# Optimization experiments

Hardware: AMD Instinct MI355X
Metric: run time of the kernel (lower is better)

The kernel has to match this reference:

```python
import jax, jax.numpy as jnp
import numpy as np

B, T, V, E, H = 256, 512, 50000, 300, 128
NORM_GAIN = 0.8     # norm_gain fed at train time
FORGET_BIAS = 1.0
EPS = 1e-12         # tf.contrib.layers.layer_norm default epsilon


def setup_inputs() -> dict:
    key = jax.random.key(0)
    k1, k2, k3 = jax.random.split(key, 3)
    x = jax.random.randint(k1, (B, T), 0, V, dtype=jnp.int32)
    embed = jax.random.normal(k2, (V, E), dtype=jnp.float32)  # tf.random_normal stddev=1
    W = jax.random.normal(k3, (E + H, 4 * H), dtype=jnp.float32) / np.float32(np.sqrt(E + H))
    gains = jnp.full((5, H), NORM_GAIN, dtype=jnp.float32)   # i, j, f, o, cell-transform
    shifts = jnp.zeros((5, H), dtype=jnp.float32)
    return {"x": x, "embed": embed, "W": W, "gains": gains, "shifts": shifts}


def _ln(v, g, b):
    # layer norm over feature axis with learned gain/shift
    m = jnp.mean(v, axis=-1, keepdims=True)
    var = jnp.mean(jnp.square(v - m), axis=-1, keepdims=True)
    return (v - m) * jax.lax.rsqrt(var + EPS) * g + b


def reference(x, embed, W, gains, shifts):
    # embedding: einsum('abc,cd->abd', one_hot(x), embed) == embed[x]
    xe = jnp.take(embed, x, axis=0)            # [B, T, E]
    xe = jnp.transpose(xe, (1, 0, 2))          # [T, B, E] for scan
    c0 = jnp.zeros((x.shape[0], H), jnp.float32)
    h0 = c0

    def step(carry, x_t):
        c, h = carry
        z = jnp.concatenate([x_t, h], axis=-1) @ W      # [B, 4H], no bias
        i, j, f, o = jnp.split(z, 4, axis=-1)
        i = _ln(i, gains[0], shifts[0])
        j = _ln(j, gains[1], shifts[1])
        f = _ln(f, gains[2], shifts[2])
        o = _ln(o, gains[3], shifts[3])
        g = jax.nn.relu(j)                              # activation=tf.nn.relu
        new_c = c * jax.nn.sigmoid(f + FORGET_BIAS) + jax.nn.sigmoid(i) * g
        new_h = jax.nn.relu(_ln(new_c, gains[4], shifts[4])) * jax.nn.sigmoid(o)
        return (new_c, new_h), new_h

    _, ys = jax.lax.scan(step, (c0, h0), xe)            # ys: [T, B, H]
    return jnp.transpose(ys, (1, 0, 2))                 # [B, T, H]
```

## Files before the change

kernel.cpp:

```cpp
#include <hip/hip_runtime.h>
#include <math.h>

#define Bb   256
#define Tt   512
#define Vv   50000
#define Ee   300
#define Hh   128
#define G4   512
#define EPS  1e-12f
#define FBIAS 1.0f

typedef _Float16 half8 __attribute__((ext_vector_type(8)));
typedef float    f32x4 __attribute__((ext_vector_type(4)));

template <int CTRL>
__device__ inline float dpp_mov(float v) {
    return __int_as_float(
        __builtin_amdgcn_update_dpp(0, __float_as_int(v), CTRL, 0xF, 0xF, true));
}
__device__ inline float red16(float v) {
    v += dpp_mov<0xB1>(v);
    v += dpp_mov<0x4E>(v);
    v += dpp_mov<0x141>(v);
    v += dpp_mov<0x140>(v);
    return v;
}
__device__ inline float red64b(float v) {
    v = red16(v);
    v += dpp_mov<0x142>(v);
    v += dpp_mov<0x143>(v);
    return __int_as_float(__builtin_amdgcn_readlane(__float_as_int(v), 63));
}

__device__ inline void lds_barrier() {
    asm volatile("s_waitcnt lgkmcnt(0)" ::: "memory");
    __builtin_amdgcn_s_barrier();
}

__device__ inline float sigm(float v) {
    return __fdividef(1.0f, 1.0f + __expf(-v));
}

#define PROJ_TILES ((Vv + 31) / 32)

__global__ __launch_bounds__(512, 2) void embed_proj_mfma(
    const float* __restrict__ embed,
    const float* __restrict__ W,
    _Float16* __restrict__ P)
{
    __shared__ __align__(16) _Float16 A[32 * 320];

    const int tid  = threadIdx.x;
    const int wv   = tid >> 6;
    const int lane = tid & 63;
    const int p16  = lane & 15;
    const int gq   = lane >> 4;

    half8 bf[4][10];
    #pragma unroll
    for (int tt = 0; tt < 4; ++tt) {
        #pragma unroll
        for (int ks = 0; ks < 10; ++ks) {
            half8 h;
            #pragma unroll
            for (int j = 0; j < 8; ++j) {
                int k = ks * 32 + gq * 8 + j;
                h[j] = (k < Ee)
                     ? (_Float16)W[(size_t)k * G4 + wv * 64 + tt * 16 + p16]
                     : (_Float16)0.f;
            }
            bf[tt][ks] = h;
        }
    }

    char* const Ab = (char*)A;
    for (int i = tid; i < 32 * 10; i += 512) {
        int row = i / 10, m = i - row * 10;
        *(uint*)(Ab + ((row * 640 + 600 + m * 4) ^ ((row & 7) << 4))) = 0u;
    }
    __syncthreads();

    for (int mtile = blockIdx.x; mtile < PROJ_TILES; mtile += gridDim.x) {
        const int r0 = mtile * 32;

        for (int i = tid; i < 32 * 75; i += 512) {
            int row = i / 75, k4 = i - row * 75;
            int grow = r0 + row;
            float4 v = (grow < Vv) ? *(const float4*)&embed[(size_t)grow * Ee + k4 * 4]
                                   : (float4){0.f, 0.f, 0.f, 0.f};
            union { _Float16 h[4]; uint2 u; } pk;
            pk.h[0] = (_Float16)v.x; pk.h[1] = (_Float16)v.y;
            pk.h[2] = (_Float16)v.z; pk.h[3] = (_Float16)v.w;
            *(uint2*)(Ab + ((row * 640 + k4 * 8) ^ ((row & 7) << 4))) = pk.u;
        }
        __syncthreads();

        f32x4 acc[2][4];
        #pragma unroll
        for (int mt = 0; mt < 2; ++mt)
            #pragma unroll
            for (int tt = 0; tt < 4; ++tt)
                acc[mt][tt] = (f32x4){0.f, 0.f, 0.f, 0.f};

        #pragma unroll
        for (int mt = 0; mt < 2; ++mt) {
            const int arow = mt * 16 + p16;
            #pragma unroll
            for (int ks = 0; ks < 10; ++ks) {
                half8 af = *(const half8*)(Ab + ((arow * 640 + ks * 64 + gq * 16)
                                                 ^ ((arow & 7) << 4)));
                #pragma unroll
                for (int tt = 0; tt < 4; ++tt)
                    acc[mt][tt] = __builtin_amdgcn_mfma_f32_16x16x32_f16(
                        af, bf[tt][ks], acc[mt][tt], 0, 0, 0);
            }
        }

        #pragma unroll
        for (int mt = 0; mt < 2; ++mt)
            #pragma unroll
            for (int tt = 0; tt < 4; ++tt)
                #pragma unroll
                for (int r = 0; r < 4; ++r) {
                    int row = r0 + mt * 16 + gq * 4 + r;
                    if (row < Vv)
                        P[(size_t)row * G4 + wv * 64 + tt * 16 + p16] =
                            (_Float16)acc[mt][tt][r];
                }
        __syncthreads();
    }
}

__global__ __launch_bounds__(128) void wsum_kernel(
    const float* __restrict__ W, float* __restrict__ Wsum)
{
    const int k = threadIdx.x;
    const float* wr = W + (size_t)(Ee + k) * G4;
    #pragma unroll
    for (int g = 0; g < 4; ++g) {
        float s = 0.f;
        for (int c = 0; c < 128; c += 4) {
            float4 v = *(const float4*)&wr[g * 128 + c];
            s += (v.x + v.y) + (v.z + v.w);
        }
        Wsum[k * 4 + g] = s;
    }
}

__global__ __launch_bounds__(256) void psum_kernel(
    const _Float16* __restrict__ P, float* __restrict__ Psum)
{
    const int lane = threadIdx.x & 63;
    const int wid  = (blockIdx.x * 256 + threadIdx.x) >> 6;
    const int nw   = (gridDim.x * 256) >> 6;
    const int g    = lane >> 4;

    for (int row = wid; row < Vv; row += nw) {
        half8 v = *(const half8*)&P[(size_t)row * G4 + lane * 8];
        float s = 0.f;
        #pragma unroll
        for (int j = 0; j < 8; ++j) s += (float)v[j];
        s = red16(s);
        if ((lane & 15) == 0) Psum[row * 4 + g] = s;
    }
}

#define RPBLK 4
#define LBLK  (Bb / RPBLK)

#define LSTM_STEP(TSTEP, PC, QC, PL, QL)                                       \
{                                                                              \
              \
    {                                                                          \
        const _Float16* pr = P + (size_t)tkR * G4;                             \
        _Pragma("unroll")                                                      \
        for (int g = 0; g < 4; ++g)                                            \
            PL[g] = *(const uint*)&pr[g * 128 + 2 * lane];                     \
        QL = *(const float4*)&Psum[(size_t)tkR * 4];                           \
    }                                                                          \
    f32x4 acc_s = (f32x4){0.f, 0.f, 0.f, 0.f};                                 \
    {                                                                          \
        half8 af[4];                                                           \
        _Pragma("unroll")                                                      \
        for (int ks = 0; ks < 4; ++ks)                                         \
            af[ks] = *(const half8*)(hb + p16 * 256 +                          \
                         ((ks * 64 + (gq << 4)) ^ ((p16 & 7) << 4)));          \
        f32x4 acc[8];                                                          \
        _Pragma("unroll")                                                      \
        for (int tt = 0; tt < 8; ++tt) acc[tt] = (f32x4){0.f, 0.f, 0.f, 0.f};  \
        _Pragma("unroll")                                                      \
        for (int tt = 0; tt < 8; ++tt) {                                       \
            _Pragma("unroll")                                                  \
            for (int ks = 0; ks < 4; ++ks)                                     \
                acc[tt] = __builtin_amdgcn_mfma_f32_16x16x32_f16(              \
                    af[ks], bfrag[tt][ks], acc[tt], 0, 0, 0);                  \
        }                                                                      \
        _Pragma("unroll")                                                      \
        for (int ks = 0; ks < 4; ++ks)                                         \
            acc_s = __builtin_amdgcn_mfma_f32_16x16x32_f16(                    \
                af[ks], bsum[ks], acc_s, 0, 0, 0);                             \
        if (lane < 16) {                                                       \
            _Pragma("unroll")                                                  \
            for (int g = 0; g < 4; ++g) {                                      \
                _Pragma("unroll")                                              \
                for (int hh = 0; hh < 2; ++hh) {                               \
                    const int tt  = g * 2 + hh;                                \
                    const int col = g * 128 + wv * 32 + hh * 16 + p16;         \
                    _Pragma("unroll")                                          \
                    for (int r = 0; r < 4; ++r) z_lds[r][col] = acc[tt][r];    \
                }                                                              \
            }                                                                  \
        }                                                                      \
    }                                                                          \
    lds_barrier();                                               \
          \
    {                                                                          \
        tkR = xtok[wv][((TSTEP) + 4 < Tt) ? (TSTEP) + 4 : Tt - 1];             \
        float2 zi[4];                                                          \
        _Pragma("unroll")                                                      \
        for (int g = 0; g < 4; ++g) {                                          \
            union { uint u; _Float16 h[2]; } pk; pk.u = PC[g];                 \
            float2 zr = *(const float2*)&z_lds[wv][g * 128 + 2 * lane];        \
            zi[g].x = zr.x + (float)pk.h[0];                                   \
            zi[g].y = zr.y + (float)pk.h[1];                                   \
        }                                                                      \
              \
        float sr = acc_s[0];                                                   \
        sr = (wv == 1) ? acc_s[1] : sr;                                        \
        sr = (wv == 2) ? acc_s[2] : sr;                                        \
        sr = (wv == 3) ? acc_s[3] : sr;                                        \
        float mean[4], rstd[4];                                                \
        {                                                                      \
            const float qs[4] = {QC.x, QC.y, QC.z, QC.w};                      \
            _Pragma("unroll")                                                  \
            for (int g = 0; g < 4; ++g) {                                      \
                float sg_ = __int_as_float(                                    \
                    __builtin_amdgcn_readlane(__float_as_int(sr), g));         \
                mean[g] = (qs[g] + sg_) * (1.0f / Hh);                         \
            }                                                                  \
        }                                                                      \
        _Pragma("unroll")                                                      \
        for (int g = 0; g < 4; ++g) {                                          \
            float q = red64b(fmaf(zi[g].x, zi[g].x, zi[g].y * zi[g].y));       \
            float var = q * (1.0f / Hh) - mean[g] * mean[g];                   \
            rstd[g] = rsqrtf(var + EPS);                                       \
        }                                                                      \
        float2 nv[4];                                                          \
        _Pragma("unroll")                                                      \
        for (int g = 0; g < 4; ++g) {                                          \
            nv[g].x = (zi[g].x - mean[g]) * rstd[g] * gg[g].x + sg[g].x;       \
            nv[g].y = (zi[g].y - mean[g]) * rstd[g] * gg[g].y + sg[g].y;       \
        }                                                                      \
        const float sox = sigm(nv[3].x);                \
        const float soy = sigm(nv[3].y);                                       \
        c0 = c0 * sigm(nv[2].x + FBIAS) + sigm(nv[0].x) * fmaxf(nv[1].x, 0.f); \
        c1 = c1 * sigm(nv[2].y + FBIAS) + sigm(nv[0].y) * fmaxf(nv[1].y, 0.f); \
        float s2 = red64b(c0 + c1);                                            \
        float q2 = red64b(fmaf(c0, c0, c1 * c1));                              \
        const float m2 = s2 * (1.0f / Hh);                                     \
        const float v2 = q2 * (1.0f / Hh) - m2 * m2;                           \
        const float r2 = rsqrtf(v2 + EPS);                                     \
        const float lc0 = (c0 - m2) * r2 * gcell.x + scell.x;                  \
        const float lc1 = (c1 - m2) * r2 * gcell.y + scell.y;                  \
        const float h0 = fmaxf(lc0, 0.f) * sox;                                \
        const float h1 = fmaxf(lc1, 0.f) * soy;                                \
        {                                                                      \
            union { _Float16 hh2[2]; uint u; } pk;                             \
            pk.hh2[0] = (_Float16)h0; pk.hh2[1] = (_Float16)h1;                \
            *(uint*)(hb + wv * 256 + ((4 * lane) ^ ((wv & 7) << 4))) = pk.u;   \
        }                                                                      \
        *(float2*)&out[((size_t)row_g * Tt + (TSTEP)) * Hh + 2 * lane] =       \
            (float2){h0, h1};                                                  \
    }                                                                          \
    lds_barrier();                                                \
}

__global__ __launch_bounds__(256, 1) void lstm_mfma6(
    const _Float16* __restrict__ P,
    const float* __restrict__ Psum,
    const float* __restrict__ Wsum,
    const float* __restrict__ W,
    const int*   __restrict__ x,
    const float* __restrict__ gains,
    const float* __restrict__ shifts,
    float* __restrict__ out)
{
    __shared__ __align__(16) float    z_lds[RPBLK][G4];
    __shared__ __align__(16) _Float16 h_lds[16][Hh];
    __shared__ __align__(16) int      xtok[RPBLK][Tt];

    const int tid  = threadIdx.x;
    const int wv   = tid >> 6;
    const int lane = tid & 63;
    const int gq   = lane >> 4;
    const int p16  = lane & 15;
    const int bb   = blockIdx.x;

    {
        const int4* xs = (const int4*)(x + (size_t)bb * RPBLK * Tt);
        int4* xd = (int4*)&xtok[0][0];
        for (int i = tid; i < 512; i += 256) xd[i] = xs[i];
    }

    {
        uint* hz = (uint*)h_lds;
        #pragma unroll
        for (int i = 0; i < 4; ++i) hz[tid + 256 * i] = 0u;
    }

    half8 bfrag[8][4];
    #pragma unroll
    for (int g = 0; g < 4; ++g) {
        #pragma unroll
        for (int hh = 0; hh < 2; ++hh) {
            #pragma unroll
            for (int ks = 0; ks < 4; ++ks) {
                half8 h;
                #pragma unroll
                for (int j = 0; j < 8; ++j) {
                    h[j] = (_Float16)W[(size_t)(Ee + ks * 32 + gq * 8 + j) * G4
                                       + g * 128 + wv * 32 + hh * 16 + p16];
                }
                bfrag[g * 2 + hh][ks] = h;
            }
        }
    }

    half8 bsum[4];
    #pragma unroll
    for (int ks = 0; ks < 4; ++ks) {
        half8 h;
        #pragma unroll
        for (int j = 0; j < 8; ++j)
            h[j] = (_Float16)Wsum[(ks * 32 + gq * 8 + j) * 4 + (p16 & 3)];
        bsum[ks] = h;
    }

    float2 gg[4], sg[4];
    #pragma unroll
    for (int g = 0; g < 4; ++g) {
        gg[g] = *(const float2*)&gains[g * Hh + 2 * lane];
        sg[g] = *(const float2*)&shifts[g * Hh + 2 * lane];
    }
    const float2 gcell = *(const float2*)&gains[4 * Hh + 2 * lane];
    const float2 scell = *(const float2*)&shifts[4 * Hh + 2 * lane];

    const int row_g = bb * RPBLK + wv;

    float c0 = 0.f, c1 = 0.f;
    char* const hb = (char*)h_lds;

    __syncthreads();

    uint pA[4], pB[4], pC[4], pD[4];
    float4 qA, qB, qC, qD;
    int tkR;
    {
        int tk0 = xtok[wv][0];
        int tk1 = xtok[wv][1];
        int tk2 = xtok[wv][2];
        tkR = xtok[wv][3];
        const _Float16* p0 = P + (size_t)tk0 * G4;
        const _Float16* p1 = P + (size_t)tk1 * G4;
        const _Float16* p2 = P + (size_t)tk2 * G4;
        #pragma unroll
        for (int g = 0; g < 4; ++g) {
            pA[g] = *(const uint*)&p0[g * 128 + 2 * lane];
            pB[g] = *(const uint*)&p1[g * 128 + 2 * lane];
            pC[g] = *(const uint*)&p2[g * 128 + 2 * lane];
        }
        qA = *(const float4*)&Psum[(size_t)tk0 * 4];
        qB = *(const float4*)&Psum[(size_t)tk1 * 4];
        qC = *(const float4*)&Psum[(size_t)tk2 * 4];
    }

    for (int t = 0; t < Tt; t += 4) {
        LSTM_STEP(t,     pA, qA, pD, qD)
        LSTM_STEP(t + 1, pB, qB, pA, qA)
        LSTM_STEP(t + 2, pC, qC, pB, qB)
        LSTM_STEP(t + 3, pD, qD, pC, qC)
    }
}

extern "C" void kernel_launch(void* const* d_in, const int* in_sizes, int n_in,
                              void* d_out, int out_size, void* d_ws, size_t ws_size,
                              hipStream_t stream) {
    const int*   x      = (const int*)d_in[0];
    const float* embed  = (const float*)d_in[1];
    const float* W      = (const float*)d_in[2];
    const float* gains  = (const float*)d_in[3];
    const float* shifts = (const float*)d_in[4];
    float* out = (float*)d_out;

    _Float16* P    = (_Float16*)d_ws;
    float*    Psum = (float*)((char*)d_ws + (size_t)Vv * G4 * 2);
    float*    Wsum = (float*)((char*)Psum + (size_t)Vv * 4 * 4);

    embed_proj_mfma<<<dim3(256), dim3(512), 0, stream>>>(embed, W, P);
    wsum_kernel<<<dim3(1), dim3(128), 0, stream>>>(W, Wsum);
    psum_kernel<<<dim3(412), dim3(256), 0, stream>>>(P, Psum);
    lstm_mfma6<<<dim3(LBLK), dim3(256), 0, stream>>>(P, Psum, Wsum, W, x,
                                                     gains, shifts, out);
}
```

Baseline: 788.6 us.

## Fuse row-sum into projection, load embed directly, split LSTM across 8 waves

The embedding projection now reads fp32 embed rows straight from global memory into MFMA fragments instead of staging them through LDS. It also computes the per-gate row sums of P in the epilogue, which removes the separate psum kernel and its re-read of P. The LSTM kernel doubles to 512 threads so each wave holds half the recurrent weight fragments and issues half the MFMAs per step. Only four waves do the elementwise cell update, and one dedicated wave computes the h·Wsum term and shares it via LDS. This shortens the per-step critical path but adds an extra LDS exchange and leaves the other four waves idle during the gate math.

```diff
diff --git a/kernel.cpp b/kernel.cpp
--- a/kernel.cpp
+++ b/kernel.cpp
@@ -41,14 +41,24 @@
     return __fdividef(1.0f, 1.0f + __expf(-v));
 }
 
+__device__ inline half8 pk8(float4 a, float4 b) {
+    half8 h;
+    h[0] = (_Float16)a.x; h[1] = (_Float16)a.y;
+    h[2] = (_Float16)a.z; h[3] = (_Float16)a.w;
+    h[4] = (_Float16)b.x; h[5] = (_Float16)b.y;
+    h[6] = (_Float16)b.z; h[7] = (_Float16)b.w;
+    return h;
+}
+
 #define PROJ_TILES ((Vv + 31) / 32)
 
-__global__ __launch_bounds__(512, 2) void embed_proj_mfma(
+__global__ __launch_bounds__(512, 2) void embed_proj2(
     const float* __restrict__ embed,
     const float* __restrict__ W,
-    _Float16* __restrict__ P)
+    _Float16* __restrict__ P,
+    float* __restrict__ Psum)
 {
-    __shared__ __align__(16) _Float16 A[32 * 320];
+    __shared__ float part[32][8];
 
     const int tid  = threadIdx.x;
     const int wv   = tid >> 6;
@@ -73,28 +83,9 @@
         }
     }
 
-    char* const Ab = (char*)A;
-    for (int i = tid; i < 32 * 10; i += 512) {
-        int row = i / 10, m = i - row * 10;
-        *(uint*)(Ab + ((row * 640 + 600 + m * 4) ^ ((row & 7) << 4))) = 0u;
-    }
-    __syncthreads();
-
     for (int mtile = blockIdx.x; mtile < PROJ_TILES; mtile += gridDim.x) {
         const int r0 = mtile * 32;
 
-        for (int i = tid; i < 32 * 75; i += 512) {
-            int row = i / 75, k4 = i - row * 75;
-            int grow = r0 + row;
-            float4 v = (grow < Vv) ? *(const float4*)&embed[(size_t)grow * Ee + k4 * 4]
-                                   : (float4){0.f, 0.f, 0.f, 0.f};
-            union { _Float16 h[4]; uint2 u; } pk;
-            pk.h[0] = (_Float16)v.x; pk.h[1] = (_Float16)v.y;
-            pk.h[2] = (_Float16)v.z; pk.h[3] = (_Float16)v.w;
-            *(uint2*)(Ab + ((row * 640 + k4 * 8) ^ ((row & 7) << 4))) = pk.u;
-        }
-        __syncthreads();
-
         f32x4 acc[2][4];
         #pragma unroll
         for (int mt = 0; mt < 2; ++mt)
@@ -104,11 +95,30 @@
 
         #pragma unroll
         for (int mt = 0; mt < 2; ++mt) {
-            const int arow = mt * 16 + p16;
+            int arow = r0 + mt * 16 + p16;
+            const float* er = embed + (size_t)(arow < Vv ? arow : Vv - 1) * Ee;
             #pragma unroll
             for (int ks = 0; ks < 10; ++ks) {
-                half8 af = *(const half8*)(Ab + ((arow * 640 + ks * 64 + gq * 16)
-                                                 ^ ((arow & 7) << 4)));
+                half8 af;
+                if (ks < 9) {
+                    const float* ep = er + ks * 32 + gq * 8;
+                    af = pk8(*(const float4*)ep, *(const float4*)(ep + 4));
+                } else {
+                    if (gq == 0) {
+                        af = pk8(*(const float4*)(er + 288),
+                                 *(const float4*)(er + 292));
+                    } else if (gq == 1) {
+                        float4 a = *(const float4*)(er + 296);
+                        af = (half8){(_Float16)a.x, (_Float16)a.y,
+                                     (_Float16)a.z, (_Float16)a.w,
+                                     (_Float16)0.f, (_Float16)0.f,
+                                     (_Float16)0.f, (_Float16)0.f};
+                    } else {
+                        af = (half8){(_Float16)0.f, (_Float16)0.f, (_Float16)0.f,
+                                     (_Float16)0.f, (_Float16)0.f, (_Float16)0.f,
+                                     (_Float16)0.f, (_Float16)0.f};
+                    }
+                }
                 #pragma unroll
                 for (int tt = 0; tt < 4; ++tt)
                     acc[mt][tt] = __builtin_amdgcn_mfma_f32_16x16x32_f16(
@@ -127,6 +137,24 @@
                         P[(size_t)row * G4 + wv * 64 + tt * 16 + p16] =
                             (_Float16)acc[mt][tt][r];
                 }
+
+        #pragma unroll
+        for (int mt = 0; mt < 2; ++mt) {
+            #pragma unroll
+            for (int r = 0; r < 4; ++r) {
+                float s = (acc[mt][0][r] + acc[mt][1][r])
+                        + (acc[mt][2][r] + acc[mt][3][r]);
+                s = red16(s);
+                if (p16 == 0) part[mt * 16 + gq * 4 + r][wv] = s;
+            }
+        }
+        __syncthreads();
+        if (tid < 128) {
+            int row = tid >> 2, g = tid & 3;
+            if (r0 + row < Vv)
+                Psum[(size_t)(r0 + row) * 4 + g] = part[row][2 * g]
+                                                 + part[row][2 * g + 1];
+        }
         __syncthreads();
     }
 }
@@ -147,74 +175,58 @@
     }
 }
 
-__global__ __launch_bounds__(256) void psum_kernel(
-    const _Float16* __restrict__ P, float* __restrict__ Psum)
-{
-    const int lane = threadIdx.x & 63;
-    const int wid  = (blockIdx.x * 256 + threadIdx.x) >> 6;
-    const int nw   = (gridDim.x * 256) >> 6;
-    const int g    = lane >> 4;
-
-    for (int row = wid; row < Vv; row += nw) {
-        half8 v = *(const half8*)&P[(size_t)row * G4 + lane * 8];
-        float s = 0.f;
-        #pragma unroll
-        for (int j = 0; j < 8; ++j) s += (float)v[j];
-        s = red16(s);
-        if ((lane & 15) == 0) Psum[row * 4 + g] = s;
-    }
-}
-
 #define RPBLK 4
 #define LBLK  (Bb / RPBLK)
 
 #define LSTM_STEP(TSTEP, PC, QC, PL, QL)                                       \
 {                                                                              \
-              \
-    {                                                                          \
+                                                        \
+    if (wv < 4) {                \
         const _Float16* pr = P + (size_t)tkR * G4;                             \
         _Pragma("unroll")                                                      \
         for (int g = 0; g < 4; ++g)                                            \
             PL[g] = *(const uint*)&pr[g * 128 + 2 * lane];                     \
         QL = *(const float4*)&Psum[(size_t)tkR * 4];                           \
     }                                                                          \
-    f32x4 acc_s = (f32x4){0.f, 0.f, 0.f, 0.f};                                 \
     {                                                                          \
         half8 af[4];                                                           \
         _Pragma("unroll")                                                      \
         for (int ks = 0; ks < 4; ++ks)                                         \
             af[ks] = *(const half8*)(hb + p16 * 256 +                          \
                          ((ks * 64 + (gq << 4)) ^ ((p16 & 7) << 4)));          \
-        f32x4 acc[8];                                                          \
-        _Pragma("unroll")                                                      \
-        for (int tt = 0; tt < 8; ++tt) acc[tt] = (f32x4){0.f, 0.f, 0.f, 0.f};  \
-        _Pragma("unroll")                                                      \
-        for (int tt = 0; tt < 8; ++tt) {                                       \
+        f32x4 acc[4];                                                          \
+        _Pragma("unroll")                                                      \
+        for (int tt = 0; tt < 4; ++tt) acc[tt] = (f32x4){0.f, 0.f, 0.f, 0.f};  \
+        _Pragma("unroll")                                                      \
+        for (int tt = 0; tt < 4; ++tt) {                                       \
             _Pragma("unroll")                                                  \
             for (int ks = 0; ks < 4; ++ks)                                     \
                 acc[tt] = __builtin_amdgcn_mfma_f32_16x16x32_f16(              \
                     af[ks], bfrag[tt][ks], acc[tt], 0, 0, 0);                  \
         }                                                                      \
-        _Pragma("unroll")                                                      \
-        for (int ks = 0; ks < 4; ++ks)                                         \
-            acc_s = __builtin_amdgcn_mfma_f32_16x16x32_f16(                    \
-                af[ks], bsum[ks], acc_s, 0, 0, 0);                             \
+        if (wv == 7) {                   \
+            f32x4 acc_s = (f32x4){0.f, 0.f, 0.f, 0.f};                         \
+            _Pragma("unroll")                                                  \
+            for (int ks = 0; ks < 4; ++ks)                                     \
+                acc_s = __builtin_amdgcn_mfma_f32_16x16x32_f16(                \
+                    af[ks], bsum[ks], acc_s, 0, 0, 0);                         \
+            if (lane < 4) {                                                    \
+                sm_lds[0][lane] = acc_s[0]; sm_lds[1][lane] = acc_s[1];        \
+                sm_lds[2][lane] = acc_s[2]; sm_lds[3][lane] = acc_s[3];        \
+            }                                                                  \
+        }                                                                      \
         if (lane < 16) {                                                       \
             _Pragma("unroll")                                                  \
-            for (int g = 0; g < 4; ++g) {                                      \
+            for (int tt = 0; tt < 4; ++tt) {                                   \
+                const int col = wv * 64 + tt * 16 + p16;                       \
                 _Pragma("unroll")                                              \
-                for (int hh = 0; hh < 2; ++hh) {                               \
-                    const int tt  = g * 2 + hh;                                \
-                    const int col = g * 128 + wv * 32 + hh * 16 + p16;         \
-                    _Pragma("unroll")                                          \
-                    for (int r = 0; r < 4; ++r) z_lds[r][col] = acc[tt][r];    \
-                }                                                              \
+                for (int r = 0; r < 4; ++r) z_lds[r][col] = acc[tt][r];        \
             }                                                                  \
         }                                                                      \
     }                                                                          \
-    lds_barrier();                                               \
-          \
-    {                                                                          \
+    lds_barrier();                                          \
+             \
+    if (wv < 4) {                                                              \
         tkR = xtok[wv][((TSTEP) + 4 < Tt) ? (TSTEP) + 4 : Tt - 1];             \
         float2 zi[4];                                                          \
         _Pragma("unroll")                                                      \
@@ -224,20 +236,14 @@
             zi[g].x = zr.x + (float)pk.h[0];                                   \
             zi[g].y = zr.y + (float)pk.h[1];                                   \
         }                                                                      \
-              \
-        float sr = acc_s[0];                                                   \
-        sr = (wv == 1) ? acc_s[1] : sr;                                        \
-        sr = (wv == 2) ? acc_s[2] : sr;                                        \
-        sr = (wv == 3) ? acc_s[3] : sr;                                        \
+        const float4 smv = *(const float4*)&sm_lds[wv][0];                     \
         float mean[4], rstd[4];                                                \
         {                                                                      \
             const float qs[4] = {QC.x, QC.y, QC.z, QC.w};                      \
+            const float sv[4] = {smv.x, smv.y, smv.z, smv.w};                  \
             _Pragma("unroll")                                                  \
-            for (int g = 0; g < 4; ++g) {                                      \
-                float sg_ = __int_as_float(                                    \
-                    __builtin_amdgcn_readlane(__float_as_int(sr), g));         \
-                mean[g] = (qs[g] + sg_) * (1.0f / Hh);                         \
-            }                                                                  \
+            for (int g = 0; g < 4; ++g)                                        \
+                mean[g] = (qs[g] + sv[g]) * (1.0f / Hh);                       \
         }                                                                      \
         _Pragma("unroll")                                                      \
         for (int g = 0; g < 4; ++g) {                                          \
@@ -251,7 +257,7 @@
             nv[g].x = (zi[g].x - mean[g]) * rstd[g] * gg[g].x + sg[g].x;       \
             nv[g].y = (zi[g].y - mean[g]) * rstd[g] * gg[g].y + sg[g].y;       \
         }                                                                      \
-        const float sox = sigm(nv[3].x);                \
+        const float sox = sigm(nv[3].x);                                       \
         const float soy = sigm(nv[3].y);                                       \
         c0 = c0 * sigm(nv[2].x + FBIAS) + sigm(nv[0].x) * fmaxf(nv[1].x, 0.f); \
         c1 = c1 * sigm(nv[2].y + FBIAS) + sigm(nv[0].y) * fmaxf(nv[1].y, 0.f); \
@@ -275,7 +281,7 @@
     lds_barrier();                                                \
 }
 
-__global__ __launch_bounds__(256, 1) void lstm_mfma6(
+__global__ __launch_bounds__(512, 1) void lstm_mfma7(
     const _Float16* __restrict__ P,
     const float* __restrict__ Psum,
     const float* __restrict__ Wsum,
@@ -288,6 +294,7 @@
     __shared__ __align__(16) float    z_lds[RPBLK][G4];
     __shared__ __align__(16) _Float16 h_lds[16][Hh];
     __shared__ __align__(16) int      xtok[RPBLK][Tt];
+    __shared__ __align__(16) float    sm_lds[4][4];
 
     const int tid  = threadIdx.x;
     const int wv   = tid >> 6;
@@ -298,42 +305,40 @@
 
     {
         const int4* xs = (const int4*)(x + (size_t)bb * RPBLK * Tt);
-        int4* xd = (int4*)&xtok[0][0];
-        for (int i = tid; i < 512; i += 256) xd[i] = xs[i];
-    }
-
+        ((int4*)&xtok[0][0])[tid] = xs[tid];
+    }
     {
         uint* hz = (uint*)h_lds;
-        #pragma unroll
-        for (int i = 0; i < 4; ++i) hz[tid + 256 * i] = 0u;
-    }
-
-    half8 bfrag[8][4];
+        hz[tid] = 0u; hz[tid + 512] = 0u;
+    }
+
+    half8 bfrag[4][4];
     #pragma unroll
-    for (int g = 0; g < 4; ++g) {
-        #pragma unroll
-        for (int hh = 0; hh < 2; ++hh) {
-            #pragma unroll
-            for (int ks = 0; ks < 4; ++ks) {
-                half8 h;
-                #pragma unroll
-                for (int j = 0; j < 8; ++j) {
-                    h[j] = (_Float16)W[(size_t)(Ee + ks * 32 + gq * 8 + j) * G4
-                                       + g * 128 + wv * 32 + hh * 16 + p16];
-                }
-                bfrag[g * 2 + hh][ks] = h;
+    for (int tt = 0; tt < 4; ++tt) {
+        #pragma unroll
+        for (int ks = 0; ks < 4; ++ks) {
+            half8 h;
+            #pragma unroll
+            for (int j = 0; j < 8; ++j) {
+                h[j] = (_Float16)W[(size_t)(Ee + ks * 32 + gq * 8 + j) * G4
+                                   + wv * 64 + tt * 16 + p16];
             }
+            bfrag[tt][ks] = h;
         }
     }
 
     half8 bsum[4];
     #pragma unroll
-    for (int ks = 0; ks < 4; ++ks) {
-        half8 h;
-        #pragma unroll
-        for (int j = 0; j < 8; ++j)
-            h[j] = (_Float16)Wsum[(ks * 32 + gq * 8 + j) * 4 + (p16 & 3)];
-        bsum[ks] = h;
+    for (int ks = 0; ks < 4; ++ks) bsum[ks] = (half8){};
+    if (wv == 7) {
+        #pragma unroll
+        for (int ks = 0; ks < 4; ++ks) {
+            half8 h;
+            #pragma unroll
+            for (int j = 0; j < 8; ++j)
+                h[j] = (_Float16)Wsum[(ks * 32 + gq * 8 + j) * 4 + (p16 & 3)];
+            bsum[ks] = h;
+        }
     }
 
     float2 gg[4], sg[4];
@@ -345,7 +350,7 @@
     const float2 gcell = *(const float2*)&gains[4 * Hh + 2 * lane];
     const float2 scell = *(const float2*)&shifts[4 * Hh + 2 * lane];
 
-    const int row_g = bb * RPBLK + wv;
+    const int row_g = bb * RPBLK + (wv & 3);
 
     float c0 = 0.f, c1 = 0.f;
     char* const hb = (char*)h_lds;
@@ -354,8 +359,8 @@
 
     uint pA[4], pB[4], pC[4], pD[4];
     float4 qA, qB, qC, qD;
-    int tkR;
-    {
+    int tkR = 0;
+    if (wv < 4) {
         int tk0 = xtok[wv][0];
         int tk1 = xtok[wv][1];
         int tk2 = xtok[wv][2];
@@ -396,9 +401,8 @@
     float*    Psum = (float*)((char*)d_ws + (size_t)Vv * G4 * 2);
     float*    Wsum = (float*)((char*)Psum + (size_t)Vv * 4 * 4);
 
-    embed_proj_mfma<<<dim3(256), dim3(512), 0, stream>>>(embed, W, P);
     wsum_kernel<<<dim3(1), dim3(128), 0, stream>>>(W, Wsum);
-    psum_kernel<<<dim3(412), dim3(256), 0, stream>>>(P, Psum);
-    lstm_mfma6<<<dim3(LBLK), dim3(256), 0, stream>>>(P, Psum, Wsum, W, x,
+    embed_proj2<<<dim3(391), dim3(512), 0, stream>>>(embed, W, P, Psum);
+    lstm_mfma7<<<dim3(LBLK), dim3(512), 0, stream>>>(P, Psum, Wsum, W, x,
                                                      gains, shifts, out);
 }
```

After: 810.0 us. +2.7%, slower.
